# Kernel optimization log

Measured on AMD Instinct MI355X. Metric: run time of the kernel, lower is better.

Reference implementation:

```python
import jax, jax.numpy as jnp
import numpy as np

HIDDEN = 300
INPUT_DIM = 300


def setup_inputs() -> dict:
    key = jax.random.key(0)
    k_in, k_wih, k_whh, k_bih, k_bhh = jax.random.split(key, 5)
    bound = 1.0 / np.sqrt(HIDDEN)  # PyTorch RNNCell init: U(-1/sqrt(H), 1/sqrt(H))
    inputs = jax.random.normal(k_in, (512, 512, INPUT_DIM), dtype=jnp.float32)
    W_ih = jax.random.uniform(k_wih, (HIDDEN, INPUT_DIM), jnp.float32, -bound, bound)
    W_hh = jax.random.uniform(k_whh, (HIDDEN, HIDDEN), jnp.float32, -bound, bound)
    b_ih = jax.random.uniform(k_bih, (HIDDEN,), jnp.float32, -bound, bound)
    b_hh = jax.random.uniform(k_bhh, (HIDDEN,), jnp.float32, -bound, bound)
    return {"inputs": inputs, "W_ih": W_ih, "W_hh": W_hh, "b_ih": b_ih, "b_hh": b_hh}


def reference(inputs, W_ih, W_hh, b_ih, b_hh):
    # inputs: [seq, batch, input_dim]; vanilla tanh RNNCell scanned over time.
    seq, bz, _ = inputs.shape
    # Precompute input projections for all timesteps in one big GEMM.
    x_proj = jnp.einsum('sbi,hi->sbh', inputs, W_ih) + b_ih + b_hh  # [seq, batch, H]

    def step(ht, xp):
        ht = jnp.tanh(xp + ht @ W_hh.T)
        return ht, None

    h0 = jnp.zeros((bz, HIDDEN), dtype=inputs.dtype)
    ht, _ = jax.lax.scan(step, h0, x_proj)
    return ht
```

## Files before the change

### kernel.cpp

```cpp
#include <hip/hip_runtime.h>
#include <hip/hip_bf16.h>


typedef unsigned short u16;
typedef unsigned int   u32;
typedef __attribute__((ext_vector_type(8)))  short bf16x8;
typedef __attribute__((ext_vector_type(4)))  short s16x4;
typedef __attribute__((ext_vector_type(4)))  float f32x4;
typedef __attribute__((ext_vector_type(16))) float f32x16;
typedef __attribute__((ext_vector_type(2)))  unsigned int u32x2;
typedef __attribute__((ext_vector_type(4)))  unsigned int u32x4;

#define HID 300
#define KP  320
#define SEQ 512
#define BZ  512
#define MTOT (SEQ*BZ)

__device__ __forceinline__ u16 f2bf(float f) {
    u32 u = __float_as_uint(f);
    return (u16)((u + 0x7FFFu + ((u >> 16) & 1u)) >> 16);
}
__device__ __forceinline__ float bf2f(u16 h) {
    return __uint_as_float((u32)h << 16);
}
__device__ __forceinline__ float tanh_fast(float x) {
    float e = __builtin_amdgcn_exp2f(x * 2.8853900817779268f);
    float r = __builtin_amdgcn_rcpf(e + 1.0f);
    return __builtin_fmaf(-2.0f, r, 1.0f);
}
__device__ __forceinline__ u32 pack2(float a, float b) {
    __hip_bfloat162 t = __float22bfloat162_rn(float2{a, b});
    return *(u32*)&t;
}
__device__ __forceinline__ void lds_barrier() {
    asm volatile("s_waitcnt lgkmcnt(0)\n\ts_barrier" ::: "memory");
}

__global__ void prep_kernel(const float* __restrict__ wih,
                            const float* __restrict__ whh,
                            const float* __restrict__ bih,
                            const float* __restrict__ bhh,
                            u16* __restrict__ wihp, u16* __restrict__ whhp,
                            float* __restrict__ bias) {
    int n = blockIdx.x, k = threadIdx.x;
    bool v = (n < HID) && (k < HID);
    int src = n * HID + k, dst = n * KP + k;
    wihp[dst] = v ? f2bf(wih[src]) : (u16)0;
    whhp[dst] = v ? f2bf(whh[src]) : (u16)0;
    if (k == 0) bias[n] = (n < HID) ? (bih[n] + bhh[n]) : 0.0f;
}

__global__ __launch_bounds__(512, 1) void xproj_kernel(
    const float* __restrict__ in, const u16* __restrict__ wihp,
    const float* __restrict__ bias, u16* __restrict__ xp) {
    __shared__ __align__(16) u16 As[2][4096];
    __shared__ __align__(16) u16 Bs[3][10240];

    const int tid = threadIdx.x;
    const int w = tid >> 6, l = tid & 63;
    const int mi = w & 3, ni = w >> 2;
    const int l31 = l & 31, l5 = l >> 5;
    const int m0 = blockIdx.x * 128;

    const int sm = tid >> 2, skg = tid & 3;

    f32x16 acc[5];
#pragma unroll
    for (int j = 0; j < 5; ++j)
#pragma unroll
        for (int r = 0; r < 16; ++r) acc[j][r] = 0.0f;

    const f32x4 zf = {0.f, 0.f, 0.f, 0.f};
    auto loadA = [&](int it, f32x4& v0, f32x4& v1) {
        int gk = it * 32 + skg * 8;
        int a0 = gk > 296 ? 296 : gk;
        int a1 = (gk + 4) > 296 ? 296 : (gk + 4);
        const float* p = in + (size_t)(m0 + sm) * HID;
        v0 = *(const f32x4*)(p + a0);
        v1 = *(const f32x4*)(p + a1);
        v0 = (gk > 296) ? zf : v0;
        v1 = ((gk + 4) > 296) ? zf : v1;
    };
    auto writeA = [&](int buf, const f32x4& v0, const f32x4& v1) {
        u32x4 pk;
        pk[0] = pack2(v0[0], v0[1]); pk[1] = pack2(v0[2], v0[3]);
        pk[2] = pack2(v1[0], v1[1]); pk[3] = pack2(v1[2], v1[3]);
        *(u32x4*)&As[buf][(skg >> 1) * 2048 + sm * 16 + (skg & 1) * 8] = pk;
    };
    auto stageB = [&](int buf, int it) {
#pragma unroll
        for (int s = 0; s < 3; ++s) {
            int i = w + 8 * s;
            if (i < 20) {
                int c = i & 3, ng = i >> 2;
                int n = ng * 64 + l;
                const u16* g = wihp + n * KP + it * 32 + c * 8;
                u16* d = &Bs[buf][c * 2560 + ng * 512];
                __builtin_amdgcn_global_load_lds(
                    (const __attribute__((address_space(1))) void*)g,
                    (__attribute__((address_space(3))) void*)d, 16, 0, 0);
            }
        }
    };

    {
        stageB(0, 0);
        f32x4 v0, v1;
        loadA(0, v0, v1);
        writeA(0, v0, v1);
        stageB(1, 1);
        asm volatile("s_waitcnt vmcnt(2)" ::: "memory");
        lds_barrier();
    }

    int cA = 0, cB = 0, sB = 2;
#pragma unroll 1
    for (int it = 0; it < 10; ++it) {
        f32x4 v0, v1;
        if (it < 9) loadA(it + 1, v0, v1);
        if (it < 8) stageB(sB, it + 2);
#pragma unroll
        for (int s = 0; s < 2; ++s) {
            bf16x8 a = *(const bf16x8*)&As[cA][s * 2048 + mi * 512 + l31 * 16 + l5 * 8];
#pragma unroll
            for (int j = 0; j < 5; ++j) {
                bf16x8 b = *(const bf16x8*)&Bs[cB][(s * 2 + l5) * 2560 + ((ni * 5 + j) * 32 + l31) * 8];
                acc[j] = __builtin_amdgcn_mfma_f32_32x32x16_bf16(a, b, acc[j], 0, 0, 0);
            }
        }
        if (it < 9) {
            writeA(cA ^ 1, v0, v1);
            if (it < 8) asm volatile("s_waitcnt vmcnt(3)" ::: "memory");
            else        asm volatile("s_waitcnt vmcnt(2)" ::: "memory");
            lds_barrier();
        }
        cA ^= 1;
        cB = (cB == 2) ? 0 : cB + 1;
        sB = (sB == 2) ? 0 : sB + 1;
    }

    const int mbase = m0 + mi * 32;
#pragma unroll
    for (int j = 0; j < 5; ++j) {
        int n = (ni * 5 + j) * 32 + l31;
        if (n < HID) {
            float bs = bias[n];
#pragma unroll
            for (int reg = 0; reg < 16; ++reg) {
                int row = (reg & 3) + 8 * (reg >> 2) + 4 * l5;
                xp[(size_t)(mbase + row) * HID + n] = f2bf(acc[j][reg] + bs);
            }
        }
    }
}

__global__ __launch_bounds__(512, 2) void rnn_recur_kernel(
    const u16* __restrict__ xp, const u16* __restrict__ whhp,
    float* __restrict__ out) {
    __shared__ __align__(16) u16 hb[2][16 * 328];

    const int tid = threadIdx.x;
    const int w = tid >> 6;
    const int l = tid & 63;
    const int br = l & 15;
    const int q  = l >> 4;
    const int b0 = blockIdx.x * 8;
    const bool t3 = (w < 4);
    const bool bv = (br < 8);

    for (int i = tid; i < (2 * 16 * 328) / 2; i += 512) ((u32*)hb)[i] = 0;

    bf16x8 Af[3][10];
#pragma unroll
    for (int j = 0; j < 3; ++j) {
        if (j < 2 || t3) {
            const int nt = w + 8 * j;
            const u16* wrow = whhp + (size_t)(nt * 16 + br) * KP;
#pragma unroll
            for (int ks = 0; ks < 10; ++ks)
                Af[j][ks] = *(const bf16x8*)(wrow + ks * 32 + q * 8);
        }
    }
#pragma unroll
    for (int j = 0; j < 3; ++j)
        if (j < 2 || t3)
#pragma unroll
            for (int ks = 0; ks < 10; ++ks)
                asm volatile("" : "+a"(Af[j][ks]));

    int xo[3];
#pragma unroll
    for (int j = 0; j < 3; ++j) {
        int n0 = (w + 8 * j) * 16 + q * 4;
        xo[j] = (n0 < HID && (j < 2 || t3) && bv) ? ((b0 + br) * HID + n0) : -1;
    }

    const s16x4 z4 = {0, 0, 0, 0};
    s16x4 xc[3], xn[3];
#pragma unroll
    for (int j = 0; j < 3; ++j) {
        xc[j] = (xo[j] >= 0) ? *(const s16x4*)(xp + xo[j]) : z4;
        xn[j] = (xo[j] >= 0) ? *(const s16x4*)(xp + (size_t)BZ * HID + xo[j]) : z4;
    }

    lds_barrier();

#pragma unroll 1
    for (int t = 0; t < SEQ; ++t) {
        const u16* hc = hb[t & 1];
        u16*       hn = hb[(t + 1) & 1];

        s16x4 xf[3];
        {
            int t2 = (t + 2 < SEQ) ? (t + 2) : (SEQ - 1);
            const u16* base = xp + (size_t)t2 * (BZ * HID);
#pragma unroll
            for (int j = 0; j < 3; ++j)
                xf[j] = (xo[j] >= 0) ? *(const s16x4*)(base + xo[j]) : z4;
        }

        f32x4 a0, a1, a2;
#pragma unroll
        for (int r = 0; r < 4; ++r) { a0[r] = 0.f; a1[r] = 0.f; a2[r] = 0.f; }

#pragma unroll
        for (int ks = 0; ks < 10; ++ks) {
            bf16x8 bfr = {0, 0, 0, 0, 0, 0, 0, 0};
            if (bv) bfr = *(const bf16x8*)&hc[br * 328 + ks * 32 + q * 8];
            a0 = __builtin_amdgcn_mfma_f32_16x16x32_bf16(Af[0][ks], bfr, a0, 0, 0, 0);
            a1 = __builtin_amdgcn_mfma_f32_16x16x32_bf16(Af[1][ks], bfr, a1, 0, 0, 0);
            if (t3)
                a2 = __builtin_amdgcn_mfma_f32_16x16x32_bf16(Af[2][ks], bfr, a2, 0, 0, 0);
        }

        {
            int n0 = w * 16 + q * 4;
            u32x2 pk;
            pk[0] = pack2(tanh_fast(a0[0] + bf2f((u16)xc[0][0])),
                          tanh_fast(a0[1] + bf2f((u16)xc[0][1])));
            pk[1] = pack2(tanh_fast(a0[2] + bf2f((u16)xc[0][2])),
                          tanh_fast(a0[3] + bf2f((u16)xc[0][3])));
            if (bv) *(u32x2*)&hn[br * 328 + n0] = pk;
        }
        {
            int n0 = (w + 8) * 16 + q * 4;
            u32x2 pk;
            pk[0] = pack2(tanh_fast(a1[0] + bf2f((u16)xc[1][0])),
                          tanh_fast(a1[1] + bf2f((u16)xc[1][1])));
            pk[1] = pack2(tanh_fast(a1[2] + bf2f((u16)xc[1][2])),
                          tanh_fast(a1[3] + bf2f((u16)xc[1][3])));
            if (bv) *(u32x2*)&hn[br * 328 + n0] = pk;
        }
        if (t3) {
            int n0 = (w + 16) * 16 + q * 4;
            u32x2 pk;
            pk[0] = pack2(tanh_fast(a2[0] + bf2f((u16)xc[2][0])),
                          tanh_fast(a2[1] + bf2f((u16)xc[2][1])));
            pk[1] = pack2(tanh_fast(a2[2] + bf2f((u16)xc[2][2])),
                          tanh_fast(a2[3] + bf2f((u16)xc[2][3])));
            if (bv) *(u32x2*)&hn[br * 328 + n0] = pk;
        }
        lds_barrier();

#pragma unroll
        for (int j = 0; j < 3; ++j) { xc[j] = xn[j]; xn[j] = xf[j]; }
    }

    const u16* hf = hb[0];
    for (int i = tid; i < 8 * HID; i += 512) {
        int r = i / HID, n = i - r * HID;
        out[(size_t)(b0 + r) * HID + n] = bf2f(hf[r * 328 + n]);
    }
}

extern "C" void kernel_launch(void* const* d_in, const int* in_sizes, int n_in,
                              void* d_out, int out_size, void* d_ws, size_t ws_size,
                              hipStream_t stream) {
    const float* in  = (const float*)d_in[0];
    const float* wih = (const float*)d_in[1];
    const float* whh = (const float*)d_in[2];
    const float* bih = (const float*)d_in[3];
    const float* bhh = (const float*)d_in[4];

    char* ws = (char*)d_ws;
    const size_t XP_BYTES = (size_t)MTOT * HID * sizeof(u16);
    u16*   xpb  = (u16*)ws;
    u16*   wihp = (u16*)(ws + XP_BYTES);
    u16*   whhp = (u16*)(ws + XP_BYTES + (size_t)KP * KP * 2);
    float* bias = (float*)(ws + XP_BYTES + 2 * (size_t)KP * KP * 2);

    prep_kernel<<<KP, KP, 0, stream>>>(wih, whh, bih, bhh, wihp, whhp, bias);
    xproj_kernel<<<MTOT / 128, 512, 0, stream>>>(in, wihp, bias, xpb);
    rnn_recur_kernel<<<BZ / 8, 512, 0, stream>>>(xpb, whhp, (float*)d_out);
}
```

Baseline: 1.124 ms.

## Fill MFMA N dimension with 16 batch rows per block and split K accumulation

Each recurrence block now processes 16 batch rows instead of 8, so the MFMA B operand no longer carries padded zero rows and the grid is halved. The x projection is loaded directly into the accumulator init, and the K reduction is split into two halves with the tanh epilogue interleaved after each tile's second half. This targets wasted MFMA lanes and per-step latency, at the cost of fewer concurrent blocks on the GPU.

```diff
diff --git a/kernel.cpp b/kernel.cpp
--- a/kernel.cpp
+++ b/kernel.cpp
@@ -165,9 +165,8 @@
     const int l = tid & 63;
     const int br = l & 15;
     const int q  = l >> 4;
-    const int b0 = blockIdx.x * 8;
+    const int b0 = blockIdx.x * 16;
     const bool t3 = (w < 4);
-    const bool bv = (br < 8);
 
     for (int i = tid; i < (2 * 16 * 328) / 2; i += 512) ((u32*)hb)[i] = 0;
 
@@ -193,7 +192,7 @@
 #pragma unroll
     for (int j = 0; j < 3; ++j) {
         int n0 = (w + 8 * j) * 16 + q * 4;
-        xo[j] = (n0 < HID && (j < 2 || t3) && bv) ? ((b0 + br) * HID + n0) : -1;
+        xo[j] = (n0 < HID && (j < 2 || t3)) ? ((b0 + br) * HID + n0) : -1;
     }
 
     const s16x4 z4 = {0, 0, 0, 0};
@@ -220,47 +219,68 @@
                 xf[j] = (xo[j] >= 0) ? *(const s16x4*)(base + xo[j]) : z4;
         }
 
-        f32x4 a0, a1, a2;
-#pragma unroll
-        for (int r = 0; r < 4; ++r) { a0[r] = 0.f; a1[r] = 0.f; a2[r] = 0.f; }
-
-#pragma unroll
-        for (int ks = 0; ks < 10; ++ks) {
-            bf16x8 bfr = {0, 0, 0, 0, 0, 0, 0, 0};
-            if (bv) bfr = *(const bf16x8*)&hc[br * 328 + ks * 32 + q * 8];
-            a0 = __builtin_amdgcn_mfma_f32_16x16x32_bf16(Af[0][ks], bfr, a0, 0, 0, 0);
-            a1 = __builtin_amdgcn_mfma_f32_16x16x32_bf16(Af[1][ks], bfr, a1, 0, 0, 0);
+        bf16x8 bL[5];
+#pragma unroll
+        for (int ks = 0; ks < 5; ++ks)
+            bL[ks] = *(const bf16x8*)&hc[br * 328 + ks * 32 + q * 8];
+
+        f32x4 a0L, a1L, a2L;
+#pragma unroll
+        for (int r = 0; r < 4; ++r) {
+            a0L[r] = bf2f((u16)xc[0][r]);
+            a1L[r] = bf2f((u16)xc[1][r]);
+            a2L[r] = bf2f((u16)xc[2][r]);
+        }
+#pragma unroll
+        for (int ks = 0; ks < 5; ++ks) {
+            a0L = __builtin_amdgcn_mfma_f32_16x16x32_bf16(Af[0][ks], bL[ks], a0L, 0, 0, 0);
+            a1L = __builtin_amdgcn_mfma_f32_16x16x32_bf16(Af[1][ks], bL[ks], a1L, 0, 0, 0);
             if (t3)
-                a2 = __builtin_amdgcn_mfma_f32_16x16x32_bf16(Af[2][ks], bfr, a2, 0, 0, 0);
-        }
-
+                a2L = __builtin_amdgcn_mfma_f32_16x16x32_bf16(Af[2][ks], bL[ks], a2L, 0, 0, 0);
+        }
+
+        bf16x8 bH[5];
+#pragma unroll
+        for (int ks = 0; ks < 5; ++ks)
+            bH[ks] = *(const bf16x8*)&hc[br * 328 + (ks + 5) * 32 + q * 8];
+
+        f32x4 a0H, a1H, a2H;
+#pragma unroll
+        for (int r = 0; r < 4; ++r) { a0H[r] = 0.f; a1H[r] = 0.f; a2H[r] = 0.f; }
+
+#pragma unroll
+        for (int ks = 0; ks < 5; ++ks)
+            a0H = __builtin_amdgcn_mfma_f32_16x16x32_bf16(Af[0][ks + 5], bH[ks], a0H, 0, 0, 0);
         {
             int n0 = w * 16 + q * 4;
             u32x2 pk;
-            pk[0] = pack2(tanh_fast(a0[0] + bf2f((u16)xc[0][0])),
-                          tanh_fast(a0[1] + bf2f((u16)xc[0][1])));
-            pk[1] = pack2(tanh_fast(a0[2] + bf2f((u16)xc[0][2])),
-                          tanh_fast(a0[3] + bf2f((u16)xc[0][3])));
-            if (bv) *(u32x2*)&hn[br * 328 + n0] = pk;
-        }
+            pk[0] = pack2(tanh_fast(a0L[0] + a0H[0]), tanh_fast(a0L[1] + a0H[1]));
+            pk[1] = pack2(tanh_fast(a0L[2] + a0H[2]), tanh_fast(a0L[3] + a0H[3]));
+            *(u32x2*)&hn[br * 328 + n0] = pk;
+        }
+
+#pragma unroll
+        for (int ks = 0; ks < 5; ++ks)
+            a1H = __builtin_amdgcn_mfma_f32_16x16x32_bf16(Af[1][ks + 5], bH[ks], a1H, 0, 0, 0);
         {
             int n0 = (w + 8) * 16 + q * 4;
             u32x2 pk;
-            pk[0] = pack2(tanh_fast(a1[0] + bf2f((u16)xc[1][0])),
-                          tanh_fast(a1[1] + bf2f((u16)xc[1][1])));
-            pk[1] = pack2(tanh_fast(a1[2] + bf2f((u16)xc[1][2])),
-                          tanh_fast(a1[3] + bf2f((u16)xc[1][3])));
-            if (bv) *(u32x2*)&hn[br * 328 + n0] = pk;
-        }
+            pk[0] = pack2(tanh_fast(a1L[0] + a1H[0]), tanh_fast(a1L[1] + a1H[1]));
+            pk[1] = pack2(tanh_fast(a1L[2] + a1H[2]), tanh_fast(a1L[3] + a1H[3]));
+            *(u32x2*)&hn[br * 328 + n0] = pk;
+        }
+
         if (t3) {
+#pragma unroll
+            for (int ks = 0; ks < 5; ++ks)
+                a2H = __builtin_amdgcn_mfma_f32_16x16x32_bf16(Af[2][ks + 5], bH[ks], a2H, 0, 0, 0);
             int n0 = (w + 16) * 16 + q * 4;
             u32x2 pk;
-            pk[0] = pack2(tanh_fast(a2[0] + bf2f((u16)xc[2][0])),
-                          tanh_fast(a2[1] + bf2f((u16)xc[2][1])));
-            pk[1] = pack2(tanh_fast(a2[2] + bf2f((u16)xc[2][2])),
-                          tanh_fast(a2[3] + bf2f((u16)xc[2][3])));
-            if (bv) *(u32x2*)&hn[br * 328 + n0] = pk;
-        }
+            pk[0] = pack2(tanh_fast(a2L[0] + a2H[0]), tanh_fast(a2L[1] + a2H[1]));
+            pk[1] = pack2(tanh_fast(a2L[2] + a2H[2]), tanh_fast(a2L[3] + a2H[3]));
+            *(u32x2*)&hn[br * 328 + n0] = pk;
+        }
+
         lds_barrier();
 
 #pragma unroll
@@ -268,7 +288,7 @@
     }
 
     const u16* hf = hb[0];
-    for (int i = tid; i < 8 * HID; i += 512) {
+    for (int i = tid; i < 16 * HID; i += 512) {
         int r = i / HID, n = i - r * HID;
         out[(size_t)(b0 + r) * HID + n] = bf2f(hf[r * 328 + n]);
     }
@@ -292,5 +312,5 @@
 
     prep_kernel<<<KP, KP, 0, stream>>>(wih, whh, bih, bhh, wihp, whhp, bias);
     xproj_kernel<<<MTOT / 128, 512, 0, stream>>>(in, wihp, bias, xpb);
-    rnn_recur_kernel<<<BZ / 8, 512, 0, stream>>>(xpb, whhp, (float*)d_out);
-}
+    rnn_recur_kernel<<<BZ / 16, 512, 0, stream>>>(xpb, whhp, (float*)d_out);
+}
```

Result: slower. 1.258 ms (+12.0%).
